# Optimization experiments

Measured on AMD Instinct MI355X. Metric: run time of the kernel, lower is better.

The kernel has to match this reference:

```python
import jax, jax.numpy as jnp
import numpy as np

N_HEAD = 16


def setup_inputs() -> dict:
    key = jax.random.key(0)
    ks = jax.random.split(key, 6)
    B, S, D = 2, 2048, 1024
    w = 0.02
    return {
        "x": jax.random.normal(ks[0], (B, S, D), dtype=jnp.float32),
        "attention_mask": jnp.ones((B, S), dtype=jnp.int32),
        "Wq": jax.random.normal(ks[1], (D, D), dtype=jnp.float32) * w,
        "bq": jnp.zeros((D,), dtype=jnp.float32),
        "Wk": jax.random.normal(ks[2], (D, D), dtype=jnp.float32) * w,
        "bk": jnp.zeros((D,), dtype=jnp.float32),
        "Wv": jax.random.normal(ks[3], (D, D), dtype=jnp.float32) * w,
        "bv": jnp.zeros((D,), dtype=jnp.float32),
        "Wp": jax.random.normal(ks[4], (D, D), dtype=jnp.float32) * w,
        "bp": jnp.zeros((D,), dtype=jnp.float32),
    }


def reference(x, attention_mask, Wq, bq, Wk, bk, Wv, bv, Wp, bp):
    # x: (B,S,D); PyTorch Linear: y = x @ W.T + b
    B, S, D = x.shape
    H = N_HEAD
    HD = D // H
    scale = 1.0 / jnp.sqrt(jnp.asarray(HD, dtype=x.dtype))

    def heads(W, b):
        return (x @ W.T + b).reshape(B, S, H, HD).transpose(0, 2, 1, 3)  # (B,H,S,HD)

    q = heads(Wq, bq)
    k = heads(Wk, bk)
    v = heads(Wv, bv)

    logits = jnp.einsum("bhsd,bhtd->bhst", q, k) * scale  # (B,H,S,S)

    causal = jnp.tril(jnp.ones((S, S), dtype=bool))  # (S,S)
    am = attention_mask.astype(bool)
    mask = causal[None, None, :, :] & (am[:, None, :, None] & am[:, None, None, :])

    float_min = jnp.finfo(x.dtype).min
    logits = jnp.where(mask, logits, float_min)
    w = jax.nn.softmax(logits, axis=-1)  # dropout is identity in eval / p=0

    attn = jnp.einsum("bhst,bhtd->bhsd", w, v)  # (B,H,S,HD)
    attn = attn.transpose(0, 2, 1, 3).reshape(B, S, D)
    return attn @ Wp.T + bp
```

## Files before the change

### kernel.cpp

```cpp
#include <hip/hip_runtime.h>


#define BB 2
#define SS 2048
#define DD 1024
#define HH 16
#define HDD 64
#define NEG_BIG (-1.0e30f)
#define QSCL 0.18033688011112042f

typedef __attribute__((ext_vector_type(8))) short short8;
typedef __attribute__((ext_vector_type(4))) float floatx4;
typedef unsigned int u32;
#define AS_GLOBAL __attribute__((address_space(1)))
#define AS_LDS    __attribute__((address_space(3)))

__device__ __forceinline__ ushort f2bf(float f) {
    unsigned u = __float_as_uint(f);
    u += 0x7fffu + ((u >> 16) & 1u);
    return (ushort)(u >> 16);
}
__device__ __forceinline__ unsigned pk2(float a, float b) {
    return ((unsigned)f2bf(b) << 16) | (unsigned)f2bf(a);
}
__device__ __forceinline__ unsigned cvtpk(float a, float b) {
    unsigned r;
    asm("v_cvt_pk_bf16_f32 %0, %1, %2" : "=v"(r) : "v"(a), "v"(b));
    return r;
}
__device__ __forceinline__ void unpack8(const uint4 u, float* d) {
    d[0] = __uint_as_float(u.x << 16);
    d[1] = __uint_as_float(u.x & 0xffff0000u);
    d[2] = __uint_as_float(u.y << 16);
    d[3] = __uint_as_float(u.y & 0xffff0000u);
    d[4] = __uint_as_float(u.z << 16);
    d[5] = __uint_as_float(u.z & 0xffff0000u);
    d[6] = __uint_as_float(u.w << 16);
    d[7] = __uint_as_float(u.w & 0xffff0000u);
}
__device__ __forceinline__ void dma16(void* lds, const void* g) {
    __builtin_amdgcn_global_load_lds((const AS_GLOBAL u32*)g, (AS_LDS u32*)lds,
                                     16, 0, 0);
}

__global__ __launch_bounds__(256) void cvt_all(
    const float* __restrict__ x, const float* __restrict__ wq,
    const float* __restrict__ wk, const float* __restrict__ wv,
    const float* __restrict__ wp,
    ushort* __restrict__ dst, ushort* __restrict__ wp_dst)
{
    const size_t flat = ((size_t)blockIdx.x * 256 + threadIdx.x) * 8;
    const float* s;
    ushort* d = dst + flat;
    size_t off;
    float scl = 1.0f;
    if (flat < (size_t)4194304)      { s = x;  off = flat; }
    else if (flat < (size_t)5242880) { s = wq; off = flat - 4194304; scl = QSCL; }
    else if (flat < (size_t)6291456) { s = wk; off = flat - 5242880; }
    else if (flat < (size_t)7340032) { s = wv; off = flat - 6291456; }
    else { s = wp; off = flat - 7340032; d = wp_dst + off; }
    const float4 a = ((const float4*)(s + off))[0];
    const float4 b = ((const float4*)(s + off))[1];
    uint4 u;
    u.x = pk2(a.x * scl, a.y * scl); u.y = pk2(a.z * scl, a.w * scl);
    u.z = pk2(b.x * scl, b.y * scl); u.w = pk2(b.z * scl, b.w * scl);
    *(uint4*)d = u;
}

__global__ __launch_bounds__(256) void gemm_qkv_wa(
    const ushort* __restrict__ A,
    const ushort* __restrict__ W0, const ushort* __restrict__ W1,
    const ushort* __restrict__ W2,
    const float* __restrict__ B0, const float* __restrict__ B1,
    const float* __restrict__ B2,
    ushort* __restrict__ O0, ushort* __restrict__ O1, ushort* __restrict__ O2)
{
    __shared__ ushort As[128 * 32];
    __shared__ ushort Bs[128 * 32];
    __shared__ float bias_s[128];

    const int z = blockIdx.z;
    const ushort* W = (z == 0) ? W0 : (z == 1 ? W1 : W2);
    const float* bias = (z == 0) ? B0 : (z == 1 ? B1 : B2);
    ushort* out = (z == 0) ? O0 : (z == 1 ? O1 : O2);
    const bool isv = (z == 2);

    const int tid = threadIdx.x;
    const int bm = blockIdx.x * 128, bn = blockIdx.y * 128;
    const int wave = tid >> 6, lane = tid & 63, quad = lane >> 4, lm = lane & 15;
    const int r0 = tid >> 2, c0 = (tid & 3) * 8;
    const int c0g = ((tid & 3) ^ ((tid >> 3) & 3)) * 8;
    const int csw8 = (quad ^ ((lm >> 1) & 3)) * 8;

    if (tid < 128) {
        float bb = bias[bn + tid];
        if (z == 0) bb *= QSCL;
        bias_s[tid] = bb;
    }

    const floatx4 zz = {0.f, 0.f, 0.f, 0.f};
    floatx4 acc[16];
#pragma unroll
    for (int i = 0; i < 16; ++i) acc[i] = zz;

    const ushort* a0 = A + (size_t)(bm + r0) * DD + c0g;
    const ushort* a1 = A + (size_t)(bm + 64 + r0) * DD + c0g;
    const ushort* w0 = W + (size_t)(bn + r0) * DD + c0g;
    const ushort* w1 = W + (size_t)(bn + 64 + r0) * DD + c0g;
    ushort* const lA0 = &As[r0 * 32 + c0];
    ushort* const lA1 = &As[(64 + r0) * 32 + c0];
    ushort* const lB0 = &Bs[r0 * 32 + c0];
    ushort* const lB1 = &Bs[(64 + r0) * 32 + c0];

    for (int k0 = 0; k0 < DD; k0 += 32) {
        __syncthreads();
        dma16(lA0, a0); dma16(lA1, a1);
        dma16(lB0, w0); dma16(lB1, w1);
        a0 += 32; a1 += 32; w0 += 32; w1 += 32;
        __syncthreads();

        if (isv) {
            const short8 bf0 = *(const short8*)&Bs[(wave * 32 + lm) * 32 + csw8];
            const short8 bf1 = *(const short8*)&Bs[(wave * 32 + 16 + lm) * 32 + csw8];
#pragma unroll
            for (int i = 0; i < 8; ++i) {
                const short8 af = *(const short8*)&As[(i * 16 + lm) * 32 + csw8];
                acc[i * 2 + 0] = __builtin_amdgcn_mfma_f32_16x16x32_bf16(
                    af, bf0, acc[i * 2 + 0], 0, 0, 0);
                acc[i * 2 + 1] = __builtin_amdgcn_mfma_f32_16x16x32_bf16(
                    af, bf1, acc[i * 2 + 1], 0, 0, 0);
            }
        } else {
            const short8 af0 = *(const short8*)&As[(wave * 32 + lm) * 32 + csw8];
            const short8 af1 = *(const short8*)&As[(wave * 32 + 16 + lm) * 32 + csw8];
#pragma unroll
            for (int j = 0; j < 8; ++j) {
                const short8 bf = *(const short8*)&Bs[(j * 16 + lm) * 32 + csw8];
                acc[j] = __builtin_amdgcn_mfma_f32_16x16x32_bf16(
                    bf, af0, acc[j], 0, 0, 0);
                acc[8 + j] = __builtin_amdgcn_mfma_f32_16x16x32_bf16(
                    bf, af1, acc[8 + j], 0, 0, 0);
            }
        }
    }

    if (isv) {
        const int b = bm >> 11, sbase = bm & 2047;
#pragma unroll
        for (int j = 0; j < 2; ++j) {
            const int n = bn + wave * 32 + j * 16 + lm;
            const float bb = bias_s[n - bn];
            ushort* orow = out + ((size_t)(b * DD + n)) * SS;
#pragma unroll
            for (int i = 0; i < 8; ++i) {
                const floatx4 a = acc[i * 2 + j];
                ushort4 v;
                v.x = f2bf(a[0] + bb); v.y = f2bf(a[1] + bb);
                v.z = f2bf(a[2] + bb); v.w = f2bf(a[3] + bb);
                *(ushort4*)(orow + sbase + i * 16 + quad * 4) = v;
            }
        }
    } else {
#pragma unroll
        for (int i = 0; i < 2; ++i) {
            const int m = bm + wave * 32 + i * 16 + lm;
            const int b = m >> 11, s = m & 2047;
#pragma unroll
            for (int j = 0; j < 8; ++j) {
                const int nl = j * 16 + quad * 4;
                const int n = bn + nl;
                const int h = n >> 6, hd = n & 63;
                const floatx4 a = acc[i * 8 + j];
                ushort4 v;
                v.x = f2bf(a[0] + bias_s[nl + 0]);
                v.y = f2bf(a[1] + bias_s[nl + 1]);
                v.z = f2bf(a[2] + bias_s[nl + 2]);
                v.w = f2bf(a[3] + bias_s[nl + 3]);
                *(ushort4*)(out + (((size_t)(b * HH + h) * SS) + s) * HDD + hd) = v;
            }
        }
    }
}

__global__ __launch_bounds__(256, 2) void gemm_proj_rs(
    const ushort* __restrict__ A, const ushort* __restrict__ W,
    const float* __restrict__ bias, float* __restrict__ out)
{
    __shared__ ushort As[128 * 32];
    __shared__ ushort Bs[128 * 32];
    __shared__ float bias_s[128];

    const int tid = threadIdx.x;
    const int bm = blockIdx.x * 128, bn = blockIdx.y * 128;
    const int wave = tid >> 6, lane = tid & 63, quad = lane >> 4, lm = lane & 15;
    const int wm = wave >> 1, wn = wave & 1;
    const int r0 = tid >> 2, c0 = (tid & 3) * 8;
    const int c0s = ((tid & 3) ^ ((tid >> 3) & 3)) * 8;
    const int csw8 = (quad ^ ((lm >> 1) & 3)) * 8;

    if (tid < 128) bias_s[tid] = bias[bn + tid];

    const floatx4 zz = {0.f, 0.f, 0.f, 0.f};
    floatx4 acc[4][4];
#pragma unroll
    for (int i = 0; i < 4; ++i)
#pragma unroll
        for (int j = 0; j < 4; ++j) acc[i][j] = zz;

    const ushort* ap = A + (size_t)(bm + r0) * DD + c0;
    const ushort* wpp = W + (size_t)(bn + r0) * DD + c0;

    uint4 ar0, ar1, wr0, wr1;
#define LOADT(K0)                                                \
    do {                                                         \
        ar0 = *(const uint4*)(ap + (K0));                        \
        ar1 = *(const uint4*)(ap + (size_t)64 * DD + (K0));      \
        wr0 = *(const uint4*)(wpp + (K0));                       \
        wr1 = *(const uint4*)(wpp + (size_t)64 * DD + (K0));     \
    } while (0)
#define STORET()                                                 \
    do {                                                         \
        *(uint4*)&As[r0 * 32 + c0s] = ar0;                       \
        *(uint4*)&As[(64 + r0) * 32 + c0s] = ar1;                \
        *(uint4*)&Bs[r0 * 32 + c0s] = wr0;                       \
        *(uint4*)&Bs[(64 + r0) * 32 + c0s] = wr1;                \
    } while (0)

    LOADT(0);
    STORET();
    __syncthreads();

    for (int k0 = 0; k0 < DD; k0 += 32) {
        const bool have_nxt = (k0 + 32) < DD;
        if (have_nxt) LOADT(k0 + 32);

        short8 af[4], bf[4];
#pragma unroll
        for (int i = 0; i < 4; ++i)
            af[i] = *(const short8*)&As[(wm * 64 + i * 16 + lm) * 32 + csw8];
#pragma unroll
        for (int j = 0; j < 4; ++j)
            bf[j] = *(const short8*)&Bs[(wn * 64 + j * 16 + lm) * 32 + csw8];
#pragma unroll
        for (int i = 0; i < 4; ++i)
#pragma unroll
            for (int j = 0; j < 4; ++j)
                acc[i][j] = __builtin_amdgcn_mfma_f32_16x16x32_bf16(
                    bf[j], af[i], acc[i][j], 0, 0, 0);

        if (have_nxt) {
            __syncthreads();
            STORET();
            __syncthreads();
        }
    }
#undef LOADT
#undef STORET

#pragma unroll
    for (int i = 0; i < 4; ++i) {
#pragma unroll
        for (int j = 0; j < 4; ++j) {
            const int nl = wn * 64 + j * 16 + quad * 4;
            const int n = bn + nl;
            const int m = bm + wm * 64 + i * 16 + lm;
            float4 v;
            v.x = acc[i][j][0] + bias_s[nl + 0];
            v.y = acc[i][j][1] + bias_s[nl + 1];
            v.z = acc[i][j][2] + bias_s[nl + 2];
            v.w = acc[i][j][3] + bias_s[nl + 3];
            *(float4*)(out + (size_t)m * DD + n) = v;
        }
    }
}

__global__ __launch_bounds__(256) void attn_mfma(
    const ushort* __restrict__ Q, const ushort* __restrict__ K,
    const ushort* __restrict__ Vt, const int* __restrict__ am,
    ushort* __restrict__ Opart, float* __restrict__ lbuf)
{
    __shared__ ushort Ks[64 * 72];
    __shared__ ushort Vts[64 * 72];
    __shared__ ushort Ps[4][16 * 72];
    __shared__ int amk_s[64];

    const int tid = threadIdx.x;
    const int wq = tid >> 6, lane = tid & 63, quad = lane >> 4, lm = lane & 15;
    const int bh = blockIdx.y, b = bh >> 4, h = bh & 15;
    const int pslot = (int)blockIdx.x;
    const int split = (int)blockIdx.z;
    const size_t base = (size_t)bh * SS * HDD;
    const size_t tbase = (size_t)bh * HDD * SS;
    const int* amrow = am + b * SS;
    const int sr = tid >> 2, sc = (tid & 3) * 16;
    const floatx4 zz = {0.f, 0.f, 0.f, 0.f};

#pragma unroll
    for (int ph = 0; ph < 2; ++ph) {
        const int qt64 = ph ? (31 - pslot) : pslot;
        const int q0 = qt64 * 64;
        const int ktend = qt64;
        const int qrow = q0 + wq * 16 + lm;

        if (ph) __syncthreads();

        short8 qf0, qf1;
        {
            const ushort* qp = Q + base + (size_t)qrow * HDD + quad * 8;
            qf0 = *(const short8*)qp;
            qf1 = *(const short8*)(qp + 32);
        }
        const int amq = amrow[qrow];
        const bool allq = __all(amq != 0);

        floatx4 o_acc[4];
#pragma unroll
        for (int n2 = 0; n2 < 4; ++n2) o_acc[n2] = zz;
        float l_lane = 0.f;

        if (split <= ktend) {
            uint4 kra, krb, vra, vrb;
            int amr = 1;
            {
                const ushort* kp = K + base + (size_t)(split * 64 + sr) * HDD + sc;
                kra = ((const uint4*)kp)[0]; krb = ((const uint4*)kp)[1];
                const ushort* vp = Vt + tbase + (size_t)sr * SS + split * 64 + sc;
                vra = ((const uint4*)vp)[0]; vrb = ((const uint4*)vp)[1];
                if (tid < 64) amr = amrow[split * 64 + tid];
            }
            *(uint4*)&Ks[sr * 72 + sc] = kra;
            *(uint4*)&Ks[sr * 72 + sc + 8] = krb;
            *(uint4*)&Vts[sr * 72 + sc] = vra;
            *(uint4*)&Vts[sr * 72 + sc + 8] = vrb;
            if (tid < 64) amk_s[tid] = amr;
            __syncthreads();

            for (int kt = split; kt <= ktend; kt += 2) {
                const int nxt = kt + 2;
                const bool have_nxt = nxt <= ktend;
                if (have_nxt) {
                    const ushort* kp = K + base + (size_t)(nxt * 64 + sr) * HDD + sc;
                    kra = ((const uint4*)kp)[0]; krb = ((const uint4*)kp)[1];
                    const ushort* vp = Vt + tbase + (size_t)sr * SS + nxt * 64 + sc;
                    vra = ((const uint4*)vp)[0]; vrb = ((const uint4*)vp)[1];
                    if (tid < 64) amr = amrow[nxt * 64 + tid];
                }

                const bool allk = (__ballot(amk_s[lane] != 0) == ~0ull);
                const bool fast = allk & allq & ((kt * 64 + 63) <= (q0 + wq * 16));
                if (fast) {
#pragma unroll
                    for (int nt = 0; nt < 4; ++nt) {
                        const short8 kf0 = *(const short8*)&Ks[(nt * 16 + lm) * 72 + quad * 8];
                        const short8 kf1 = *(const short8*)&Ks[(nt * 16 + lm) * 72 + 32 + quad * 8];
                        floatx4 s = zz;
                        s = __builtin_amdgcn_mfma_f32_16x16x32_bf16(kf0, qf0, s, 0, 0, 0);
                        s = __builtin_amdgcn_mfma_f32_16x16x32_bf16(kf1, qf1, s, 0, 0, 0);
                        const float e0 = exp2f(fminf(s[0], 40.f));
                        const float e1 = exp2f(fminf(s[1], 40.f));
                        const float e2 = exp2f(fminf(s[2], 40.f));
                        const float e3 = exp2f(fminf(s[3], 40.f));
                        l_lane += (e0 + e1) + (e2 + e3);
                        uint2 pv;
                        pv.x = cvtpk(e0, e1); pv.y = cvtpk(e2, e3);
                        *(uint2*)&Ps[wq][lm * 72 + nt * 16 + quad * 4] = pv;
                    }
                } else {
#pragma unroll
                    for (int nt = 0; nt < 4; ++nt) {
                        const short8 kf0 = *(const short8*)&Ks[(nt * 16 + lm) * 72 + quad * 8];
                        const short8 kf1 = *(const short8*)&Ks[(nt * 16 + lm) * 72 + 32 + quad * 8];
                        const int4 amk4 = *(const int4*)&amk_s[nt * 16 + quad * 4];
                        floatx4 s = zz;
                        s = __builtin_amdgcn_mfma_f32_16x16x32_bf16(kf0, qf0, s, 0, 0, 0);
                        s = __builtin_amdgcn_mfma_f32_16x16x32_bf16(kf1, qf1, s, 0, 0, 0);
                        const int t0 = kt * 64 + nt * 16 + quad * 4;
                        const bool mq = amq != 0;
                        const bool ok0 = amk4.x && mq && (t0 + 0 <= qrow);
                        const bool ok1 = amk4.y && mq && (t0 + 1 <= qrow);
                        const bool ok2 = amk4.z && mq && (t0 + 2 <= qrow);
                        const bool ok3 = amk4.w && mq && (t0 + 3 <= qrow);
                        const float e0 = exp2f(fminf(ok0 ? s[0] : NEG_BIG, 40.f));
                        const float e1 = exp2f(fminf(ok1 ? s[1] : NEG_BIG, 40.f));
                        const float e2 = exp2f(fminf(ok2 ? s[2] : NEG_BIG, 40.f));
                        const float e3 = exp2f(fminf(ok3 ? s[3] : NEG_BIG, 40.f));
                        l_lane += (e0 + e1) + (e2 + e3);
                        uint2 pv;
                        pv.x = cvtpk(e0, e1); pv.y = cvtpk(e2, e3);
                        *(uint2*)&Ps[wq][lm * 72 + nt * 16 + quad * 4] = pv;
                    }
                }

                const short8 af0 = *(const short8*)&Ps[wq][lm * 72 + quad * 8];
                const short8 af1 = *(const short8*)&Ps[wq][lm * 72 + 32 + quad * 8];
#pragma unroll
                for (int n2 = 0; n2 < 4; ++n2) {
                    const short8 vf0 = *(const short8*)&Vts[(n2 * 16 + lm) * 72 + quad * 8];
                    const short8 vf1 = *(const short8*)&Vts[(n2 * 16 + lm) * 72 + 32 + quad * 8];
                    o_acc[n2] = __builtin_amdgcn_mfma_f32_16x16x32_bf16(
                        vf0, af0, o_acc[n2], 0, 0, 0);
                    o_acc[n2] = __builtin_amdgcn_mfma_f32_16x16x32_bf16(
                        vf1, af1, o_acc[n2], 0, 0, 0);
                }

                if (have_nxt) {
                    __syncthreads();
                    *(uint4*)&Ks[sr * 72 + sc] = kra;
                    *(uint4*)&Ks[sr * 72 + sc + 8] = krb;
                    *(uint4*)&Vts[sr * 72 + sc] = vra;
                    *(uint4*)&Vts[sr * 72 + sc + 8] = vrb;
                    if (tid < 64) amk_s[tid] = amr;
                    __syncthreads();
                }
            }
        }

        float l = l_lane;
        l += __shfl_xor(l, 16);
        l += __shfl_xor(l, 32);
        if (quad == 0)
            lbuf[(size_t)split * (BB * HH * SS) + (size_t)bh * SS + qrow] = l;
#pragma unroll
        for (int n2 = 0; n2 < 4; ++n2) {
            uint2 v;
            v.x = cvtpk(o_acc[n2][0], o_acc[n2][1]);
            v.y = cvtpk(o_acc[n2][2], o_acc[n2][3]);
            *(uint2*)(Opart + (size_t)split * (BB * SS * DD)
                        + ((size_t)(b * SS + qrow)) * DD + h * HDD + n2 * 16 + quad * 4) = v;
        }
    }
}

__global__ __launch_bounds__(256) void combine(
    const ushort* __restrict__ Opart, const float* __restrict__ lbuf,
    ushort* __restrict__ Aout)
{
    const size_t e = ((size_t)blockIdx.x * 256 + threadIdx.x) * 8;
    const int m = (int)(e >> 10);
    const int col = (int)(e & 1023);
    const int b = m >> 11, s = m & 2047, h = col >> 6;
    const float l = lbuf[(b * HH + h) * SS + s]
                  + lbuf[BB * HH * SS + (b * HH + h) * SS + s];
    const float inv = l > 0.f ? 1.f / l : 0.f;
    const uint4 u0 = *(const uint4*)(Opart + e);
    const uint4 u1 = *(const uint4*)(Opart + (size_t)BB * SS * DD + e);
    float f0[8], f1[8];
    unpack8(u0, f0);
    unpack8(u1, f1);
    uint4 o;
    o.x = pk2((f0[0] + f1[0]) * inv, (f0[1] + f1[1]) * inv);
    o.y = pk2((f0[2] + f1[2]) * inv, (f0[3] + f1[3]) * inv);
    o.z = pk2((f0[4] + f1[4]) * inv, (f0[5] + f1[5]) * inv);
    o.w = pk2((f0[6] + f1[6]) * inv, (f0[7] + f1[7]) * inv);
    *(uint4*)(Aout + e) = o;
}

extern "C" void kernel_launch(void* const* d_in, const int* in_sizes, int n_in,
                              void* d_out, int out_size, void* d_ws, size_t ws_size,
                              hipStream_t stream) {
    const float* x  = (const float*)d_in[0];
    const int*   am = (const int*)d_in[1];
    const float* Wq = (const float*)d_in[2];
    const float* bq = (const float*)d_in[3];
    const float* Wk = (const float*)d_in[4];
    const float* bk = (const float*)d_in[5];
    const float* Wv = (const float*)d_in[6];
    const float* bv = (const float*)d_in[7];
    const float* Wp = (const float*)d_in[8];
    const float* bp = (const float*)d_in[9];
    float* out = (float*)d_out;

    const size_t elems = (size_t)BB * HH * SS * HDD;
    ushort* q_ws = (ushort*)d_ws;
    ushort* k_ws = q_ws + elems;
    ushort* v_ws = k_ws + elems;
    float*  lbuf = (float*)(v_ws + elems);
    ushort* wpb  = (ushort*)(lbuf + 2 * BB * HH * SS);

    ushort* xb  = (ushort*)d_out;
    ushort* wqb = xb + 4194304;
    ushort* wkb = wqb + 1048576;
    ushort* wvb = wkb + 1048576;

    cvt_all<<<4096, 256, 0, stream>>>(x, Wq, Wk, Wv, Wp, xb, wpb);

    gemm_qkv_wa<<<dim3(32, 8, 3), 256, 0, stream>>>(
        xb, wqb, wkb, wvb, bq, bk, bv, q_ws, k_ws, v_ws);

    attn_mfma<<<dim3(16, BB * HH, 2), 256, 0, stream>>>(
        q_ws, k_ws, v_ws, am, (ushort*)d_out, lbuf);

    combine<<<2048, 256, 0, stream>>>((const ushort*)d_out, lbuf, q_ws);

    gemm_proj_rs<<<dim3(32, 8), 256, 0, stream>>>(q_ws, wpb, bp, out);
}
```

Baseline: 216.0 us.

## Double-buffer LDS in QKV and projection GEMMs with register prefetch

Both GEMM kernels now use two LDS buffers with register-staged global prefetch. Global loads for later K-tiles are issued before the current tile's MFMAs, and each step needs one barrier instead of two. The QKV GEMM switches from direct global-to-LDS DMA to register loads with swizzled LDS stores and asks for 3 blocks per CU. The attention kernel also drops the fminf clamp before exp2f, which saves ALU work but removes the guard against overflow on large logits.

Result: slower. 250.4 us (+15.9%).

```diff
diff --git a/kernel.cpp b/kernel.cpp
--- a/kernel.cpp
+++ b/kernel.cpp
@@ -41,6 +41,11 @@
 __device__ __forceinline__ void dma16(void* lds, const void* g) {
     __builtin_amdgcn_global_load_lds((const AS_GLOBAL u32*)g, (AS_LDS u32*)lds,
                                      16, 0, 0);
+}
+__device__ __forceinline__ void bar() {
+    asm volatile("s_waitcnt lgkmcnt(0)" ::: "memory");
+    __builtin_amdgcn_s_barrier();
+    asm volatile("" ::: "memory");
 }
 
 __global__ __launch_bounds__(256) void cvt_all(
@@ -67,7 +72,7 @@
     *(uint4*)d = u;
 }
 
-__global__ __launch_bounds__(256) void gemm_qkv_wa(
+__global__ __launch_bounds__(256, 3) void gemm_qkv_t34(
     const ushort* __restrict__ A,
     const ushort* __restrict__ W0, const ushort* __restrict__ W1,
     const ushort* __restrict__ W2,
@@ -75,8 +80,8 @@
     const float* __restrict__ B2,
     ushort* __restrict__ O0, ushort* __restrict__ O1, ushort* __restrict__ O2)
 {
-    __shared__ ushort As[128 * 32];
-    __shared__ ushort Bs[128 * 32];
+    __shared__ ushort As[2][128 * 32];
+    __shared__ ushort Bs[2][128 * 32];
     __shared__ float bias_s[128];
 
     const int z = blockIdx.z;
@@ -89,7 +94,7 @@
     const int bm = blockIdx.x * 128, bn = blockIdx.y * 128;
     const int wave = tid >> 6, lane = tid & 63, quad = lane >> 4, lm = lane & 15;
     const int r0 = tid >> 2, c0 = (tid & 3) * 8;
-    const int c0g = ((tid & 3) ^ ((tid >> 3) & 3)) * 8;
+    const int c0s = ((tid & 3) ^ ((tid >> 3) & 3)) * 8;
     const int csw8 = (quad ^ ((lm >> 1) & 3)) * 8;
 
     if (tid < 128) {
@@ -103,46 +108,70 @@
 #pragma unroll
     for (int i = 0; i < 16; ++i) acc[i] = zz;
 
-    const ushort* a0 = A + (size_t)(bm + r0) * DD + c0g;
-    const ushort* a1 = A + (size_t)(bm + 64 + r0) * DD + c0g;
-    const ushort* w0 = W + (size_t)(bn + r0) * DD + c0g;
-    const ushort* w1 = W + (size_t)(bn + 64 + r0) * DD + c0g;
-    ushort* const lA0 = &As[r0 * 32 + c0];
-    ushort* const lA1 = &As[(64 + r0) * 32 + c0];
-    ushort* const lB0 = &Bs[r0 * 32 + c0];
-    ushort* const lB1 = &Bs[(64 + r0) * 32 + c0];
-
-    for (int k0 = 0; k0 < DD; k0 += 32) {
-        __syncthreads();
-        dma16(lA0, a0); dma16(lA1, a1);
-        dma16(lB0, w0); dma16(lB1, w1);
-        a0 += 32; a1 += 32; w0 += 32; w1 += 32;
-        __syncthreads();
-
-        if (isv) {
-            const short8 bf0 = *(const short8*)&Bs[(wave * 32 + lm) * 32 + csw8];
-            const short8 bf1 = *(const short8*)&Bs[(wave * 32 + 16 + lm) * 32 + csw8];
-#pragma unroll
-            for (int i = 0; i < 8; ++i) {
-                const short8 af = *(const short8*)&As[(i * 16 + lm) * 32 + csw8];
-                acc[i * 2 + 0] = __builtin_amdgcn_mfma_f32_16x16x32_bf16(
-                    af, bf0, acc[i * 2 + 0], 0, 0, 0);
-                acc[i * 2 + 1] = __builtin_amdgcn_mfma_f32_16x16x32_bf16(
-                    af, bf1, acc[i * 2 + 1], 0, 0, 0);
-            }
-        } else {
-            const short8 af0 = *(const short8*)&As[(wave * 32 + lm) * 32 + csw8];
-            const short8 af1 = *(const short8*)&As[(wave * 32 + 16 + lm) * 32 + csw8];
-#pragma unroll
-            for (int j = 0; j < 8; ++j) {
-                const short8 bf = *(const short8*)&Bs[(j * 16 + lm) * 32 + csw8];
-                acc[j] = __builtin_amdgcn_mfma_f32_16x16x32_bf16(
-                    bf, af0, acc[j], 0, 0, 0);
-                acc[8 + j] = __builtin_amdgcn_mfma_f32_16x16x32_bf16(
-                    bf, af1, acc[8 + j], 0, 0, 0);
-            }
-        }
+    const ushort* ap = A + (size_t)(bm + r0) * DD + c0;
+    const ushort* wpp = W + (size_t)(bn + r0) * DD + c0;
+
+    uint4 pA0, pA1, pA2, pA3, pB0, pB1, pB2, pB3;
+
+#define LOADS(s, K0)                                              \
+    do {                                                          \
+        s##0 = *(const uint4*)(ap + (K0));                        \
+        s##1 = *(const uint4*)(ap + (size_t)64 * DD + (K0));      \
+        s##2 = *(const uint4*)(wpp + (K0));                       \
+        s##3 = *(const uint4*)(wpp + (size_t)64 * DD + (K0));     \
+    } while (0)
+#define STORES(buf, s)                                            \
+    do {                                                          \
+        *(uint4*)&As[buf][r0 * 32 + c0s] = s##0;                  \
+        *(uint4*)&As[buf][(64 + r0) * 32 + c0s] = s##1;           \
+        *(uint4*)&Bs[buf][r0 * 32 + c0s] = s##2;                  \
+        *(uint4*)&Bs[buf][(64 + r0) * 32 + c0s] = s##3;           \
+    } while (0)
+#define COMPUTE(buf)                                                          \
+    do {                                                                      \
+        if (isv) {                                                            \
+            const short8 bf0 = *(const short8*)&Bs[buf][(wave * 32 + lm) * 32 + csw8];      \
+            const short8 bf1 = *(const short8*)&Bs[buf][(wave * 32 + 16 + lm) * 32 + csw8]; \
+            _Pragma("unroll")                                                 \
+            for (int i = 0; i < 8; ++i) {                                     \
+                const short8 af = *(const short8*)&As[buf][(i * 16 + lm) * 32 + csw8];      \
+                acc[i * 2 + 0] = __builtin_amdgcn_mfma_f32_16x16x32_bf16(     \
+                    af, bf0, acc[i * 2 + 0], 0, 0, 0);                        \
+                acc[i * 2 + 1] = __builtin_amdgcn_mfma_f32_16x16x32_bf16(     \
+                    af, bf1, acc[i * 2 + 1], 0, 0, 0);                        \
+            }                                                                 \
+        } else {                                                              \
+            const short8 af0 = *(const short8*)&As[buf][(wave * 32 + lm) * 32 + csw8];      \
+            const short8 af1 = *(const short8*)&As[buf][(wave * 32 + 16 + lm) * 32 + csw8]; \
+            _Pragma("unroll")                                                 \
+            for (int j = 0; j < 8; ++j) {                                     \
+                const short8 bf = *(const short8*)&Bs[buf][(j * 16 + lm) * 32 + csw8];      \
+                acc[j] = __builtin_amdgcn_mfma_f32_16x16x32_bf16(             \
+                    bf, af0, acc[j], 0, 0, 0);                                \
+                acc[8 + j] = __builtin_amdgcn_mfma_f32_16x16x32_bf16(         \
+                    bf, af1, acc[8 + j], 0, 0, 0);                            \
+            }                                                                 \
+        }                                                                     \
+    } while (0)
+
+    LOADS(pA, 0);
+    STORES(0, pA);
+    bar();
+    LOADS(pA, 32);
+
+    for (int k0 = 0; k0 < DD; k0 += 64) {
+        if (k0 + 64 < DD) LOADS(pB, k0 + 64);
+        COMPUTE(0);
+        STORES(1, pA);
+        bar();
+        if (k0 + 96 < DD) LOADS(pA, k0 + 96);
+        COMPUTE(1);
+        if (k0 + 64 < DD) STORES(0, pB);
+        bar();
     }
+#undef LOADS
+#undef STORES
+#undef COMPUTE
 
     if (isv) {
         const int b = bm >> 11, sbase = bm & 2047;
@@ -182,12 +211,12 @@
     }
 }
 
-__global__ __launch_bounds__(256, 2) void gemm_proj_rs(
+__global__ __launch_bounds__(256, 2) void gemm_proj_t34(
     const ushort* __restrict__ A, const ushort* __restrict__ W,
     const float* __restrict__ bias, float* __restrict__ out)
 {
-    __shared__ ushort As[128 * 32];
-    __shared__ ushort Bs[128 * 32];
+    __shared__ ushort As[2][128 * 32];
+    __shared__ ushort Bs[2][128 * 32];
     __shared__ float bias_s[128];
 
     const int tid = threadIdx.x;
@@ -210,52 +239,57 @@
     const ushort* ap = A + (size_t)(bm + r0) * DD + c0;
     const ushort* wpp = W + (size_t)(bn + r0) * DD + c0;
 
-    uint4 ar0, ar1, wr0, wr1;
-#define LOADT(K0)                                                \
-    do {                                                         \
-        ar0 = *(const uint4*)(ap + (K0));                        \
-        ar1 = *(const uint4*)(ap + (size_t)64 * DD + (K0));      \
-        wr0 = *(const uint4*)(wpp + (K0));                       \
-        wr1 = *(const uint4*)(wpp + (size_t)64 * DD + (K0));     \
+    uint4 pA0, pA1, pA2, pA3, pB0, pB1, pB2, pB3;
+
+#define LOADS(s, K0)                                              \
+    do {                                                          \
+        s##0 = *(const uint4*)(ap + (K0));                        \
+        s##1 = *(const uint4*)(ap + (size_t)64 * DD + (K0));      \
+        s##2 = *(const uint4*)(wpp + (K0));                       \
+        s##3 = *(const uint4*)(wpp + (size_t)64 * DD + (K0));     \
     } while (0)
-#define STORET()                                                 \
-    do {                                                         \
-        *(uint4*)&As[r0 * 32 + c0s] = ar0;                       \
-        *(uint4*)&As[(64 + r0) * 32 + c0s] = ar1;                \
-        *(uint4*)&Bs[r0 * 32 + c0s] = wr0;                       \
-        *(uint4*)&Bs[(64 + r0) * 32 + c0s] = wr1;                \
+#define STORES(buf, s)                                            \
+    do {                                                          \
+        *(uint4*)&As[buf][r0 * 32 + c0s] = s##0;                  \
+        *(uint4*)&As[buf][(64 + r0) * 32 + c0s] = s##1;           \
+        *(uint4*)&Bs[buf][r0 * 32 + c0s] = s##2;                  \
+        *(uint4*)&Bs[buf][(64 + r0) * 32 + c0s] = s##3;           \
     } while (0)
-
-    LOADT(0);
-    STORET();
-    __syncthreads();
-
-    for (int k0 = 0; k0 < DD; k0 += 32) {
-        const bool have_nxt = (k0 + 32) < DD;
-        if (have_nxt) LOADT(k0 + 32);
-
-        short8 af[4], bf[4];
-#pragma unroll
-        for (int i = 0; i < 4; ++i)
-            af[i] = *(const short8*)&As[(wm * 64 + i * 16 + lm) * 32 + csw8];
-#pragma unroll
-        for (int j = 0; j < 4; ++j)
-            bf[j] = *(const short8*)&Bs[(wn * 64 + j * 16 + lm) * 32 + csw8];
-#pragma unroll
-        for (int i = 0; i < 4; ++i)
-#pragma unroll
-            for (int j = 0; j < 4; ++j)
-                acc[i][j] = __builtin_amdgcn_mfma_f32_16x16x32_bf16(
-                    bf[j], af[i], acc[i][j], 0, 0, 0);
-
-        if (have_nxt) {
-            __syncthreads();
-            STORET();
-            __syncthreads();
-        }
+#define COMPUTE(buf)                                                          \
+    do {                                                                      \
+        short8 af[4], bf[4];                                                  \
+        _Pragma("unroll")                                                     \
+        for (int i = 0; i < 4; ++i)                                           \
+            af[i] = *(const short8*)&As[buf][(wm * 64 + i * 16 + lm) * 32 + csw8]; \
+        _Pragma("unroll")                                                     \
+        for (int j = 0; j < 4; ++j)                                           \
+            bf[j] = *(const short8*)&Bs[buf][(wn * 64 + j * 16 + lm) * 32 + csw8]; \
+        _Pragma("unroll")                                                     \
+        for (int i = 0; i < 4; ++i)                                           \
+            _Pragma("unroll")                                                 \
+            for (int j = 0; j < 4; ++j)                                       \
+                acc[i][j] = __builtin_amdgcn_mfma_f32_16x16x32_bf16(          \
+                    bf[j], af[i], acc[i][j], 0, 0, 0);                        \
+    } while (0)
+
+    LOADS(pA, 0);
+    STORES(0, pA);
+    bar();
+    LOADS(pA, 32);
+
+    for (int k0 = 0; k0 < DD; k0 += 64) {
+        if (k0 + 64 < DD) LOADS(pB, k0 + 64);
+        COMPUTE(0);
+        STORES(1, pA);
+        bar();
+        if (k0 + 96 < DD) LOADS(pA, k0 + 96);
+        COMPUTE(1);
+        if (k0 + 64 < DD) STORES(0, pB);
+        bar();
     }
-#undef LOADT
-#undef STORET
+#undef LOADS
+#undef STORES
+#undef COMPUTE
 
 #pragma unroll
     for (int i = 0; i < 4; ++i) {
@@ -356,10 +390,10 @@
                         floatx4 s = zz;
                         s = __builtin_amdgcn_mfma_f32_16x16x32_bf16(kf0, qf0, s, 0, 0, 0);
                         s = __builtin_amdgcn_mfma_f32_16x16x32_bf16(kf1, qf1, s, 0, 0, 0);
-                        const float e0 = exp2f(fminf(s[0], 40.f));
-                        const float e1 = exp2f(fminf(s[1], 40.f));
-                        const float e2 = exp2f(fminf(s[2], 40.f));
-                        const float e3 = exp2f(fminf(s[3], 40.f));
+                        const float e0 = exp2f(s[0]);
+                        const float e1 = exp2f(s[1]);
+                        const float e2 = exp2f(s[2]);
+                        const float e3 = exp2f(s[3]);
                         l_lane += (e0 + e1) + (e2 + e3);
                         uint2 pv;
                         pv.x = cvtpk(e0, e1); pv.y = cvtpk(e2, e3);
@@ -380,10 +414,10 @@
                         const bool ok1 = amk4.y && mq && (t0 + 1 <= qrow);
                         const bool ok2 = amk4.z && mq && (t0 + 2 <= qrow);
                         const bool ok3 = amk4.w && mq && (t0 + 3 <= qrow);
-                        const float e0 = exp2f(fminf(ok0 ? s[0] : NEG_BIG, 40.f));
-                        const float e1 = exp2f(fminf(ok1 ? s[1] : NEG_BIG, 40.f));
-                        const float e2 = exp2f(fminf(ok2 ? s[2] : NEG_BIG, 40.f));
-                        const float e3 = exp2f(fminf(ok3 ? s[3] : NEG_BIG, 40.f));
+                        const float e0 = exp2f(ok0 ? s[0] : NEG_BIG);
+                        const float e1 = exp2f(ok1 ? s[1] : NEG_BIG);
+                        const float e2 = exp2f(ok2 ? s[2] : NEG_BIG);
+                        const float e3 = exp2f(ok3 ? s[3] : NEG_BIG);
                         l_lane += (e0 + e1) + (e2 + e3);
                         uint2 pv;
                         pv.x = cvtpk(e0, e1); pv.y = cvtpk(e2, e3);
@@ -484,7 +518,7 @@
 
     cvt_all<<<4096, 256, 0, stream>>>(x, Wq, Wk, Wv, Wp, xb, wpb);
 
-    gemm_qkv_wa<<<dim3(32, 8, 3), 256, 0, stream>>>(
+    gemm_qkv_t34<<<dim3(32, 8, 3), 256, 0, stream>>>(
         xb, wqb, wkb, wvb, bq, bk, bv, q_ws, k_ws, v_ws);
 
     attn_mfma<<<dim3(16, BB * HH, 2), 256, 0, stream>>>(
@@ -492,5 +526,5 @@
 
     combine<<<2048, 256, 0, stream>>>((const ushort*)d_out, lbuf, q_ws);
 
-    gemm_proj_rs<<<dim3(32, 8), 256, 0, stream>>>(q_ws, wpb, bp, out);
-}
+    gemm_proj_t34<<<dim3(32, 8), 256, 0, stream>>>(q_ws, wpb, bp, out);
+}
```
